# Performance work log

Measured on AMD Instinct MI355X. Metric: run time of the kernel, lower is better.

Reference implementation:

```python
import jax, jax.numpy as jnp
import numpy as np

B = 131072
D = 64
NUM_REL = 32


def setup_inputs() -> dict:
    key = jax.random.key(0)
    k1, k2, k3, k4 = jax.random.split(key, 4)
    embeds1 = jax.random.normal(k1, (B, D), dtype=jnp.float32)
    embeds2 = jax.random.normal(k2, (B, D), dtype=jnp.float32)
    rels = jax.random.randint(k3, (B,), 0, NUM_REL, dtype=jnp.int32)
    # learned relation table: one D*D matrix per relation type
    rel_embeds = jax.random.normal(k4, (NUM_REL, D * D), dtype=jnp.float32)
    return {"embeds1": embeds1, "embeds2": embeds2, "rels": rels,
            "rel_embeds": rel_embeds}


def reference(embeds1, embeds2, rels, rel_embeds):
    # gather per-sample relation matrices: [B, D, D]
    rel_mats = rel_embeds[rels].reshape(-1, D, D)
    # per-sample bilinear form: score_b = e1_b^T R_b e2_b  -> [B]
    e1R = jnp.einsum("bd,bde->be", embeds1, rel_mats)
    return (e1R * embeds2).sum(axis=1)
```

## Files before the change

kernel.cpp:

```cpp
#include <hip/hip_runtime.h>
#include <hip/hip_bf16.h>
#include <cstddef>

#define BB 131072
#define DD 64
#define NREL 32

#define CAP 4608
#define WPB (CAP / 64)
#define PERM_SLOTS (NREL * CAP)

#define SCB 256
#define SCT 512
#define CSTRIDE 16

typedef __attribute__((ext_vector_type(8))) __bf16 bf16x8;
typedef __attribute__((ext_vector_type(16))) float f32x16;

__global__ __launch_bounds__(SCT) void scatter_atomic(
    const int* __restrict__ rels, int* __restrict__ cursor,
    int* __restrict__ perm) {
  __shared__ int hist[NREL];
  __shared__ int base[NREL];
  const int t = threadIdx.x;
  if (t < NREL) hist[t] = 0;
  __syncthreads();
  const int s = blockIdx.x * SCT + t;
  const int rv = rels[s];
  const int rank = atomicAdd(&hist[rv], 1);
  __syncthreads();
  if (t < NREL) base[t] = atomicAdd(&cursor[t * CSTRIDE], hist[t]);
  __syncthreads();
  perm[rv * CAP + base[rv] + rank] = s;
}

__global__ __launch_bounds__(64) void bilinear_mfma(
    const float* __restrict__ e1g, const float* __restrict__ e2g,
    const float* __restrict__ relE, const int* __restrict__ perm,
    const int* __restrict__ cursor, float* __restrict__ out) {
  __shared__ float sP[64 * 33];
  const int lane = threadIdx.x;
  const int r0 = blockIdx.y;
  const int end = cursor[r0 * CSTRIDE];
  const int s0i = blockIdx.x * 64;
  if (s0i >= end) return;
  const int slot = s0i + lane;
  const bool valid = slot < end;
  const int pk = perm[r0 * CAP + slot] & 0x1FFFF;
  const int h = lane >> 5;
  const int l31 = lane & 31;
  const int rowid0 = __shfl(pk, l31);
  const int rowid1 = __shfl(pk, 32 + l31);

  const float* __restrict__ R = relE + (size_t)r0 * (DD * DD);

  f32x16 acc[2][2];
#pragma unroll
  for (int ti = 0; ti < 2; ++ti)
#pragma unroll
    for (int tj = 0; tj < 2; ++tj)
#pragma unroll
      for (int i = 0; i < 16; ++i) acc[ti][tj][i] = 0.f;

#pragma unroll
  for (int kc = 0; kc < 4; ++kc) {
    bf16x8 aH[2], aL[2], bH[2], bL[2];
#pragma unroll
    for (int ti = 0; ti < 2; ++ti) {
      const float* ap =
          e1g + (size_t)(ti ? rowid1 : rowid0) * DD + kc * 16 + 8 * h;
      const float4 x0 = *(const float4*)(ap);
      const float4 x1 = *(const float4*)(ap + 4);
      const float xs[8] = {x0.x, x0.y, x0.z, x0.w, x1.x, x1.y, x1.z, x1.w};
#pragma unroll
      for (int j = 0; j < 8; ++j) {
        const __bf16 hb = (__bf16)xs[j];
        aH[ti][j] = hb;
        aL[ti][j] = (__bf16)(xs[j] - (float)hb);
      }
    }
#pragma unroll
    for (int tj = 0; tj < 2; ++tj) {
      const float* q = R + (size_t)(kc * 16 + 8 * h) * DD + 32 * tj + l31;
#pragma unroll
      for (int j = 0; j < 8; ++j) {
        const float x = q[(size_t)j * DD];
        const __bf16 hb = (__bf16)x;
        bH[tj][j] = hb;
        bL[tj][j] = (__bf16)(x - (float)hb);
      }
    }
#pragma unroll
    for (int ti = 0; ti < 2; ++ti)
#pragma unroll
      for (int tj = 0; tj < 2; ++tj) {
        acc[ti][tj] = __builtin_amdgcn_mfma_f32_32x32x16_bf16(aH[ti], bH[tj], acc[ti][tj], 0, 0, 0);
        acc[ti][tj] = __builtin_amdgcn_mfma_f32_32x32x16_bf16(aH[ti], bL[tj], acc[ti][tj], 0, 0, 0);
        acc[ti][tj] = __builtin_amdgcn_mfma_f32_32x32x16_bf16(aL[ti], bH[tj], acc[ti][tj], 0, 0, 0);
      }
  }

#pragma unroll
  for (int ti = 0; ti < 2; ++ti)
#pragma unroll
    for (int g = 0; g < 4; ++g)
#pragma unroll
      for (int q = 0; q < 4; ++q) {
        const int reg = g * 4 + q;
        const int rbase = 32 * ti + q + 8 * g;
        const int s0 = __builtin_amdgcn_readlane(pk, rbase);
        const int s1 = __builtin_amdgcn_readlane(pk, rbase + 4);
        const int bs = h ? s1 : s0;
        const float* er = e2g + (size_t)bs * DD + l31;
        const float v = fmaf(acc[ti][0][reg], er[0], acc[ti][1][reg] * er[32]);
        sP[(rbase + 4 * h) * 33 + l31] = v;
      }
  __syncthreads();
  float sc = 0.f;
#pragma unroll
  for (int c = 0; c < 32; ++c) sc += sP[lane * 33 + c];
  if (valid) out[pk] = sc;
}

extern "C" void kernel_launch(void* const* d_in, const int* in_sizes, int n_in,
                              void* d_out, int out_size, void* d_ws, size_t ws_size,
                              hipStream_t stream) {
  const float* e1 = (const float*)d_in[0];
  const float* e2 = (const float*)d_in[1];
  const int* rels = (const int*)d_in[2];
  const float* relE = (const float*)d_in[3];
  float* out = (float*)d_out;

  int* perm = (int*)d_ws;
  int* cursor = perm + PERM_SLOTS;

  hipMemsetAsync(cursor, 0, NREL * CSTRIDE * sizeof(int), stream);
  scatter_atomic<<<SCB, SCT, 0, stream>>>(rels, cursor, perm);
  bilinear_mfma<<<dim3(WPB, NREL), 64, 0, stream>>>(e1, e2, relE, perm, cursor,
                                                    out);
}
```

Baseline: 122.8 us.

## Stage relation matrix as split bf16 in LDS shared by four waves per block

Each block now runs four waves (256 threads) on four consecutive 64-sample tiles of one relation. The block loads the relation matrix once, splits it into hi/lo bf16, and stores it transposed in padded LDS. Each wave then reads its B fragments with vector LDS loads instead of doing strided global loads and conversions itself. This cuts redundant global traffic and conversion work on R, in exchange for an extra barrier, more LDS per block, and blocks where some waves have no valid samples.

```diff
diff --git a/kernel.cpp b/kernel.cpp
--- a/kernel.cpp
+++ b/kernel.cpp
@@ -7,12 +7,15 @@
 #define NREL 32
 
 #define CAP 4608
-#define WPB (CAP / 64)
+#define TILES (CAP / 64)
+#define BLKX (TILES / 4)
 #define PERM_SLOTS (NREL * CAP)
 
 #define SCB 256
 #define SCT 512
 #define CSTRIDE 16
+
+#define RSTR 72
 
 typedef __attribute__((ext_vector_type(8))) __bf16 bf16x8;
 typedef __attribute__((ext_vector_type(16))) float f32x16;
@@ -34,25 +37,47 @@
   perm[rv * CAP + base[rv] + rank] = s;
 }
 
-__global__ __launch_bounds__(64) void bilinear_mfma(
+__global__ __launch_bounds__(256, 4) void bilinear_mfma(
     const float* __restrict__ e1g, const float* __restrict__ e2g,
     const float* __restrict__ relE, const int* __restrict__ perm,
     const int* __restrict__ cursor, float* __restrict__ out) {
-  __shared__ float sP[64 * 33];
-  const int lane = threadIdx.x;
+  __shared__ float smem[4 * 64 * 33];
+  __bf16* RH = (__bf16*)smem;
+  __bf16* RL = RH + 64 * RSTR;
+  const int t = threadIdx.x;
   const int r0 = blockIdx.y;
   const int end = cursor[r0 * CSTRIDE];
-  const int s0i = blockIdx.x * 64;
-  if (s0i >= end) return;
-  const int slot = s0i + lane;
+  const int tile0 = blockIdx.x * 4;
+  if (tile0 * 64 >= end) return;
+
+  const int wid = t >> 6;
+  const int lane = t & 63;
+  const int h = lane >> 5;
+  const int l31 = lane & 31;
+  const int slot = (tile0 + wid) * 64 + lane;
   const bool valid = slot < end;
   const int pk = perm[r0 * CAP + slot] & 0x1FFFF;
-  const int h = lane >> 5;
-  const int l31 = lane & 31;
   const int rowid0 = __shfl(pk, l31);
   const int rowid1 = __shfl(pk, 32 + l31);
 
-  const float* __restrict__ R = relE + (size_t)r0 * (DD * DD);
+  {
+    const float* Rg = relE + (size_t)r0 * (DD * DD);
+    const int k = t >> 2;
+    const int n0 = (t & 3) * 16;
+    float4 x[4];
+#pragma unroll
+    for (int i = 0; i < 4; ++i)
+      x[i] = *(const float4*)(Rg + (size_t)k * DD + n0 + 4 * i);
+    const float* xs = (const float*)x;
+#pragma unroll
+    for (int j = 0; j < 16; ++j) {
+      const float v = xs[j];
+      const __bf16 hb = (__bf16)v;
+      RH[(n0 + j) * RSTR + k] = hb;
+      RL[(n0 + j) * RSTR + k] = (__bf16)(v - (float)hb);
+    }
+  }
+  __syncthreads();
 
   f32x16 acc[2][2];
 #pragma unroll
@@ -81,14 +106,9 @@
     }
 #pragma unroll
     for (int tj = 0; tj < 2; ++tj) {
-      const float* q = R + (size_t)(kc * 16 + 8 * h) * DD + 32 * tj + l31;
-#pragma unroll
-      for (int j = 0; j < 8; ++j) {
-        const float x = q[(size_t)j * DD];
-        const __bf16 hb = (__bf16)x;
-        bH[tj][j] = hb;
-        bL[tj][j] = (__bf16)(x - (float)hb);
-      }
+      const int bo = (32 * tj + l31) * RSTR + kc * 16 + 8 * h;
+      bH[tj] = *(const bf16x8*)(RH + bo);
+      bL[tj] = *(const bf16x8*)(RL + bo);
     }
 #pragma unroll
     for (int ti = 0; ti < 2; ++ti)
@@ -100,6 +120,9 @@
       }
   }
 
+  __syncthreads();
+
+  float* sP = smem + wid * (64 * 33);
 #pragma unroll
   for (int ti = 0; ti < 2; ++ti)
 #pragma unroll
@@ -136,6 +159,6 @@
 
   hipMemsetAsync(cursor, 0, NREL * CSTRIDE * sizeof(int), stream);
   scatter_atomic<<<SCB, SCT, 0, stream>>>(rels, cursor, perm);
-  bilinear_mfma<<<dim3(WPB, NREL), 64, 0, stream>>>(e1, e2, relE, perm, cursor,
-                                                    out);
+  bilinear_mfma<<<dim3(BLKX, NREL), 256, 0, stream>>>(e1, e2, relE, perm,
+                                                      cursor, out);
 }
```

New measurement: 113.5 us. 1.08x faster.
